# Kernel tuning notes

Measured on AMD Instinct MI355X. Metric: run time of the kernel, lower is better.

The kernel has to match this reference:

```python
import jax, jax.numpy as jnp
import numpy as np

L = 32      # num_layer
N_ORD = 64  # order_of_a_LTImodel
U = 64      # u_size
Y = 64      # y_size
T = 8192    # sequence length
SCALE = 0.05  # keep block-bidiagonal A spectrally stable over 8192 steps


def setup_inputs() -> dict:
    key = jax.random.key(0)
    k_u, k_a, k_b0, k_bl, k_c = jax.random.split(key, 5)
    inp = {
        "input": jax.random.normal(k_u, (T, U), dtype=jnp.float32),
        # per-layer A_i weights (diagonal blocks)
        "A_stack": jax.random.normal(k_a, (L, N_ORD, N_ORD), dtype=jnp.float32) * SCALE,
        # layer-0 B (maps u -> state)
        "B0": jax.random.normal(k_b0, (N_ORD, U), dtype=jnp.float32) * SCALE,
        # layer i>=1 B weights (sub-diagonal coupling blocks)
        "B_lower": jax.random.normal(k_bl, (L - 1, N_ORD, N_ORD), dtype=jnp.float32) * SCALE,
        # per-layer C_i weights, concatenated along columns in forward
        "C_stack": jax.random.normal(k_c, (L, Y, N_ORD), dtype=jnp.float32),
        # D is frozen zeros (feedthrough=False)
        "D_w": jnp.zeros((Y, U), dtype=jnp.float32),
    }
    return inp


def _assemble(A_stack, B0, B_lower, C_stack):
    l, n, _ = A_stack.shape
    S = l * n
    A = jnp.zeros((S, S), A_stack.dtype)
    for i in range(l):  # fixed small structural loop
        A = A.at[i * n:(i + 1) * n, i * n:(i + 1) * n].set(A_stack[i])
    for i in range(1, l):
        A = A.at[i * n:(i + 1) * n, (i - 1) * n:i * n].set(B_lower[i - 1])
    B = jnp.concatenate([B0, jnp.zeros((S - n, B0.shape[1]), B0.dtype)], axis=0)
    # torch.cat([C_i], dim=1): [Y, L*n]
    C = jnp.transpose(C_stack, (1, 0, 2)).reshape(C_stack.shape[1], S)
    return A, B, C


def reference(input, A_stack, B0, B_lower, C_stack, D_w):
    A, B, C = _assemble(A_stack, B0, B_lower, C_stack)
    S = A.shape[0]
    x0 = jnp.zeros((S,), input.dtype)

    def step(x, u):
        y = C @ x + D_w @ u      # output BEFORE state update (y_t uses x_t)
        x_next = A @ x + B @ u
        return x_next, y

    _, ys = jax.lax.scan(step, x0, input)
    return ys  # [T, Y]
```

## Files before the change

### kernel.cpp

```cpp
#include <hip/hip_runtime.h>


#define LYR 32
#define NO  64
#define TSEQ 8192
#define JT  16
#define KD  (JT*NO)
#define PROWS (TSEQ+JT)
#define PBUF ((size_t)PROWS*NO)
#define FD  4

typedef _Float16 h16;
typedef _Float16 h16x8 __attribute__((ext_vector_type(8)));
typedef float    f32x4 __attribute__((ext_vector_type(4)));

__global__ __launch_bounds__(256) void prep1(
    const float* __restrict__ u, const float* __restrict__ B0,
    const float* __restrict__ Bl, const float* __restrict__ Cst,
    h16* __restrict__ pall, h16* __restrict__ ccast, float* __restrict__ kf32)
{
    const int n_pad0 = JT*NO;
    const int n_u    = TSEQ*NO;
    const int n_c    = LYR*NO*NO;
    const int n_k    = LYR*NO*NO;
    const int n_zp   = 32*JT*NO;
    const int total8 = (n_pad0 + n_u + n_c + n_k + n_zp) >> 3;
    int idx8 = blockIdx.x*256 + threadIdx.x;
    const int4 zero4 = make_int4(0,0,0,0);
    for (; idx8 < total8; idx8 += gridDim.x*256) {
        int e = idx8 << 3;
        if (e < n_pad0) { *(int4*)&pall[e] = zero4; continue; }
        e -= n_pad0;
        if (e < n_u) {
            f32x4 f0 = *(const f32x4*)&u[e];
            f32x4 f1 = *(const f32x4*)&u[e+4];
            h16 ov[8];
            #pragma unroll
            for (int j = 0; j < 4; j++) { ov[j] = (h16)f0[j]; ov[4+j] = (h16)f1[j]; }
            *(int4*)&pall[n_pad0 + e] = *(int4*)&ov[0];
            continue;
        }
        e -= n_u;
        if (e < n_c) {
            f32x4 f0 = *(const f32x4*)&Cst[e];
            f32x4 f1 = *(const f32x4*)&Cst[e+4];
            h16 ov[8];
            #pragma unroll
            for (int j = 0; j < 4; j++) { ov[j] = (h16)f0[j]; ov[4+j] = (h16)f1[j]; }
            *(int4*)&ccast[e] = *(int4*)&ov[0];
            continue;
        }
        e -= n_c;
        if (e < n_k) {
            int i = e >> 12;
            int r = e & 4095;
            const float* src = (i == 0) ? &B0[r] : &Bl[e - 4096];
            float* dst = &kf32[((size_t)i*JT)*4096 + r];
            *(f32x4*)&dst[0] = *(const f32x4*)&src[0];
            *(f32x4*)&dst[4] = *(const f32x4*)&src[4];
            continue;
        }
        e -= n_k;
        int b = e >> 10;
        int off = e & 1023;
        *(int4*)&pall[(size_t)(b+1)*PBUF + off] = zero4;
    }
}

__global__ __launch_bounds__(256) void build_step(
    const float* __restrict__ A_stack, float* __restrict__ kf32,
    float* __restrict__ apow, int s)
{
    int h = 1 << s;
    int extra = (s < 3) ? 1 : 0;
    int slots = h + extra;
    int layer = blockIdx.x / slots;
    int q     = blockIdx.x % slots;
    const float* X = (s == 0) ? (A_stack + (size_t)layer*4096)
                              : (apow + ((size_t)layer*4 + (s-1))*4096);
    const float* Yop;
    float* Z;
    if (q < h) { Yop = kf32 + ((size_t)layer*JT + q)*4096;
                 Z   = kf32 + ((size_t)layer*JT + h + q)*4096; }
    else       { Yop = X;
                 Z   = apow + ((size_t)layer*4 + s)*4096; }

    __shared__ float lx[64*68];
    __shared__ float ly[64*68];
    int tid = threadIdx.x;
    for (int e = tid; e < 4096; e += 256) {
        int r = e >> 6, c = e & 63;
        lx[r*68 + c] = X[e];
        ly[r*68 + c] = Yop[e];
    }
    __syncthreads();
    int r0 = (tid >> 4) << 2;
    int c0 = (tid & 15) << 2;
    float acc[4][4] = {};
    for (int k = 0; k < 64; k++) {
        float a0 = lx[(r0+0)*68 + k];
        float a1 = lx[(r0+1)*68 + k];
        float a2 = lx[(r0+2)*68 + k];
        float a3 = lx[(r0+3)*68 + k];
        f32x4 bv = *(const f32x4*)&ly[k*68 + c0];
        #pragma unroll
        for (int j = 0; j < 4; j++) {
            acc[0][j] += a0*bv[j]; acc[1][j] += a1*bv[j];
            acc[2][j] += a2*bv[j]; acc[3][j] += a3*bv[j];
        }
    }
    #pragma unroll
    for (int i2 = 0; i2 < 4; i2++) {
        f32x4 o; o[0]=acc[i2][0]; o[1]=acc[i2][1]; o[2]=acc[i2][2]; o[3]=acc[i2][3];
        *(f32x4*)&Z[(size_t)(r0+i2)*64 + c0] = o;
    }
}

__global__ __launch_bounds__(256) void castK(const float* __restrict__ kf32,
                                             h16* __restrict__ kt)
{
    int idx4 = blockIdx.x*256 + threadIdx.x;
    const int total4 = (LYR*NO*KD) >> 2;
    for (; idx4 < total4; idx4 += gridDim.x*256) {
        int idx = idx4 << 2;
        int i   = idx >> 16;
        int rem = idx & 65535;
        int n   = rem >> 10;
        int kap = rem & 1023;
        int jp  = kap >> 6, m = kap & 63;
        int j   = JT-1-jp;
        f32x4 f = *(const f32x4*)&kf32[(((size_t)i*JT + j)*64 + n)*64 + m];
        h16 ov[4];
        #pragma unroll
        for (int t = 0; t < 4; t++) ov[t] = (h16)f[t];
        *(int2*)&kt[idx] = *(int2*)&ov[0];
    }
}

template<int S>
__device__ __forceinline__ void phase_body(
    const h16* inb, h16* outb, const h16* __restrict__ kb,
    h16* __restrict__ gout, const int w0, float* red, const int tid)
{
    const int wv = tid >> 6, lane = tid & 63, r = lane & 15, q = lane >> 4;
    const h16* abase = inb + (r + wv*4)*72 + q*8;
    const h16* bbase = kb + (size_t)r*KD + wv*256 + q*8;
#define LDA(s, ls) (*(const h16x8*)(abase + ((s)*16 + ((ls)>>1))*72 + ((ls)&1)*32))
#define LDB(c, ls) (*(const h16x8*)(bbase + (c)*(16*KD) + (ls)*32))
    f32x4 acc[S][4] = {};
    h16x8 a[2][S], b[4][4];
    #pragma unroll
    for (int ls = 0; ls < 2; ls++)
        #pragma unroll
        for (int s = 0; s < S; s++) a[ls][s] = LDA(s, ls);
    #pragma unroll
    for (int ls = 0; ls < 4; ls++)
        #pragma unroll
        for (int c = 0; c < 4; c++) b[ls][c] = LDB(c, ls);
    #pragma unroll
    for (int ls = 0; ls < 8; ls++) {
        h16x8 ca[S], cb[4];
        #pragma unroll
        for (int s = 0; s < S; s++) ca[s] = a[ls&1][s];
        #pragma unroll
        for (int c = 0; c < 4; c++) cb[c] = b[ls&3][c];
        if (ls < 6) {
            #pragma unroll
            for (int s = 0; s < S; s++) a[ls&1][s] = LDA(s, ls+2);
        }
        if (ls < 4) {
            #pragma unroll
            for (int c = 0; c < 4; c++) b[ls&3][c] = LDB(c, ls+4);
        }
        #pragma unroll
        for (int s = 0; s < S; s++)
            #pragma unroll
            for (int c = 0; c < 4; c++)
                acc[s][c] = __builtin_amdgcn_mfma_f32_16x16x32_f16(ca[s], cb[c], acc[s][c], 0,0,0);
    }
#undef LDA
#undef LDB
    const int cb2 = (tid & 7) << 3;
    #pragma unroll
    for (int ch = 0; ch < (S+2)/3; ch++) {
        const int sbase = ch*3;
        const int nt = (S - sbase) < 3 ? (S - sbase) : 3;
        __syncthreads();
        if (wv >= 2) {
            float* myred = red + (size_t)(wv-2)*(48*68);
            #pragma unroll
            for (int s2 = 0; s2 < 3; s2++) if (s2 < nt)
                #pragma unroll
                for (int c = 0; c < 4; c++)
                    #pragma unroll
                    for (int g = 0; g < 4; g++)
                        myred[(s2*16 + q*4 + g)*68 + c*16 + r] = acc[sbase+s2][c][g];
        }
        __syncthreads();
        if (wv < 2) {
            float* myred = red + (size_t)wv*(48*68);
            #pragma unroll
            for (int s2 = 0; s2 < 3; s2++) if (s2 < nt)
                #pragma unroll
                for (int c = 0; c < 4; c++)
                    #pragma unroll
                    for (int g = 0; g < 4; g++)
                        myred[(s2*16 + q*4 + g)*68 + c*16 + r] += acc[sbase+s2][c][g];
        }
        __syncthreads();
        for (int w = tid >> 3; w < nt*16; w += 32) {
            f32x4 u0 = *(const f32x4*)&red[w*68 + cb2];
            f32x4 u1 = *(const f32x4*)&red[w*68 + cb2 + 4];
            f32x4 v0 = *(const f32x4*)&red[48*68 + w*68 + cb2];
            f32x4 v1 = *(const f32x4*)&red[48*68 + w*68 + cb2 + 4];
            u0 += v0; u1 += v1;
            h16 ov[8];
            #pragma unroll
            for (int j = 0; j < 4; j++) { ov[j] = (h16)u0[j]; ov[4+j] = (h16)u1[j]; }
            const int W = sbase*16 + w;
            if (outb) *(int4*)&outb[W*72 + cb2] = *(int4*)&ov[0];
            const unsigned wrel = (unsigned)(W - w0);
            if (wrel < 32u) *(int4*)&gout[(size_t)wrel*64 + cb2] = *(int4*)&ov[0];
        }
    }
    __syncthreads();
}

__global__ __launch_bounds__(256) void stage4(
    h16* pall, const h16* __restrict__ kt, int i0)
{
    __shared__ __align__(16) h16   bufA[96*72];
    __shared__ __align__(16) h16   bufB[96*72];
    __shared__ __align__(16) float red[2*48*68];
    const int tid = threadIdx.x;
    const size_t t0 = (size_t)blockIdx.x * 32;

    const h16* pin = pall + (size_t)i0*PBUF;
    for (int e = tid; e < 96*8; e += 256) {
        int rr = e >> 3, cc = e & 7;
        long g = (long)t0 - 48 + rr;
        int4 v = make_int4(0,0,0,0);
        if (g >= 0) v = *(const int4*)&pin[(size_t)g*64 + cc*8];
        *(int4*)&bufA[rr*72 + cc*8] = v;
    }
    __syncthreads();

    h16* g1 = pall + (size_t)(i0+1)*PBUF + (JT + t0)*64;
    h16* g2 = pall + (size_t)(i0+2)*PBUF + (JT + t0)*64;
    h16* g3 = pall + (size_t)(i0+3)*PBUF + (JT + t0)*64;
    h16* g4 = pall + (size_t)(i0+4)*PBUF + (JT + t0)*64;
    const h16* k1 = kt + (size_t)(i0+0)*NO*KD;
    const h16* k2 = kt + (size_t)(i0+1)*NO*KD;
    const h16* k3 = kt + (size_t)(i0+2)*NO*KD;
    const h16* k4 = kt + (size_t)(i0+3)*NO*KD;

    phase_body<5>(bufA, bufB, k1, g1, 48, red, tid);
    phase_body<4>(bufB, bufA, k2, g2, 32, red, tid);
    phase_body<3>(bufA, bufB, k3, g3, 16, red, tid);
    phase_body<2>(bufB, (h16*)0, k4, g4, 0, red, tid);
}

__global__ __launch_bounds__(256, 2) void y_final(
    const h16* __restrict__ pall, const h16* __restrict__ ccast,
    float* __restrict__ out)
{
    __shared__ __align__(16) float red[2*32*68];
    int tid = threadIdx.x;
    size_t t0 = (size_t)blockIdx.x * 32;
    int wv = tid >> 6, lane = tid & 63, r = lane & 15, q = lane >> 4;
    const h16* abase = pall + (size_t)(wv*8 + 1)*PBUF + (JT + t0 + r)*64 + q*8;
    const h16* bbase = ccast + (size_t)(wv*8)*4096 + (size_t)r*64 + q*8;
#define LDA2(s, ls) (*(const h16x8*)(abase + (size_t)((ls)>>1)*PBUF + (s)*(16*64) + ((ls)&1)*32))
#define LDB2(c, ls) (*(const h16x8*)(bbase + ((ls)>>1)*4096 + (c)*(16*64) + ((ls)&1)*32))
    f32x4 acc[2][4] = {};
    h16x8 a[4][2], b[4][4];
    #pragma unroll
    for (int ls = 0; ls < 4; ls++) {
        #pragma unroll
        for (int s = 0; s < 2; s++) a[ls][s] = LDA2(s, ls);
        #pragma unroll
        for (int c = 0; c < 4; c++) b[ls][c] = LDB2(c, ls);
    }
    #pragma unroll
    for (int ls = 0; ls < 16; ls++) {
        h16x8 ca[2], cb[4];
        #pragma unroll
        for (int s = 0; s < 2; s++) ca[s] = a[ls&3][s];
        #pragma unroll
        for (int c = 0; c < 4; c++) cb[c] = b[ls&3][c];
        if (ls < 12) {
            #pragma unroll
            for (int s = 0; s < 2; s++) a[ls&3][s] = LDA2(s, ls+4);
            #pragma unroll
            for (int c = 0; c < 4; c++) b[ls&3][c] = LDB2(c, ls+4);
        }
        #pragma unroll
        for (int s = 0; s < 2; s++)
            #pragma unroll
            for (int c = 0; c < 4; c++)
                acc[s][c] = __builtin_amdgcn_mfma_f32_16x16x32_f16(ca[s], cb[c], acc[s][c], 0,0,0);
    }
#undef LDA2
#undef LDB2
    if (wv >= 2) {
        float* myred = red + (size_t)(wv-2)*(32*68);
        #pragma unroll
        for (int s = 0; s < 2; s++)
            #pragma unroll
            for (int c = 0; c < 4; c++)
                #pragma unroll
                for (int g = 0; g < 4; g++)
                    myred[(s*16 + q*4 + g)*68 + c*16 + r] = acc[s][c][g];
    }
    __syncthreads();
    if (wv < 2) {
        float* myred = red + (size_t)wv*(32*68);
        #pragma unroll
        for (int s = 0; s < 2; s++)
            #pragma unroll
            for (int c = 0; c < 4; c++)
                #pragma unroll
                for (int g = 0; g < 4; g++)
                    myred[(s*16 + q*4 + g)*68 + c*16 + r] += acc[s][c][g];
    }
    __syncthreads();
    int orow = tid >> 3, cb2 = (tid & 7) << 3;
    f32x4 u0 = *(const f32x4*)&red[orow*68 + cb2];
    f32x4 u1 = *(const f32x4*)&red[orow*68 + cb2 + 4];
    f32x4 v0 = *(const f32x4*)&red[32*68 + orow*68 + cb2];
    f32x4 v1 = *(const f32x4*)&red[32*68 + orow*68 + cb2 + 4];
    u0 += v0; u1 += v1;
    size_t obase = (t0 + orow)*64 + cb2;
    *(f32x4*)&out[obase]     = u0;
    *(f32x4*)&out[obase + 4] = u1;
}

extern "C" void kernel_launch(void* const* d_in, const int* in_sizes, int n_in,
                              void* d_out, int out_size, void* d_ws, size_t ws_size,
                              hipStream_t stream)
{
    const float* u   = (const float*)d_in[0];
    const float* Ast = (const float*)d_in[1];
    const float* B0  = (const float*)d_in[2];
    const float* Bl  = (const float*)d_in[3];
    const float* Cst = (const float*)d_in[4];
    float* out = (float*)d_out;
    (void)in_sizes; (void)n_in; (void)out_size; (void)ws_size;

    char* ws = (char*)d_ws;
    const size_t PBUF_BYTES = PBUF*sizeof(h16);
    h16*   pall  = (h16*)ws;
    h16*   ccast = (h16*)(ws + 33*PBUF_BYTES);
    h16*   kt    = (h16*)(ws + 33*PBUF_BYTES + 262144);
    float* kf32  = (float*)(ws + 33*PBUF_BYTES + 262144 + 4194304);
    float* apow  = (float*)(ws + 33*PBUF_BYTES + 262144 + 4194304 + 8388608);

    prep1<<<512, 256, 0, stream>>>(u, B0, Bl, Cst, pall, ccast, kf32);
    for (int s = 0; s < 4; s++) {
        int h = 1 << s;
        int grid = 32*(h + (s < 3 ? 1 : 0));
        build_step<<<grid, 256, 0, stream>>>(Ast, kf32, apow, s);
    }
    castK<<<2048, 256, 0, stream>>>(kf32, kt);
    for (int i = 0; i < LYR; i += FD) {
        stage4<<<TSEQ/32, 256, 0, stream>>>(pall, kt, i);
    }
    y_final<<<TSEQ/32, 256, 0, stream>>>(pall, ccast, out);
}
```

Baseline: 306.9 us.

## Halve time tile per block and fuse fp16 K-cast into last power step

Stage4 and y_final now process 16 timesteps per block instead of 32, doubling the grid, shrinking LDS buffers, and adding a two-blocks-per-SM launch bound so more waves stay resident. The fp16 cast and reversal of the impulse-response blocks moves into the final build_step launch, which removes the separate castK kernel. The catch is that the 48-row halo is now recomputed relative to a smaller useful tile, so redundant MFMA work per output row rises.

```diff
diff --git a/kernel.cpp b/kernel.cpp
--- a/kernel.cpp
+++ b/kernel.cpp
@@ -69,7 +69,7 @@
 
 __global__ __launch_bounds__(256) void build_step(
     const float* __restrict__ A_stack, float* __restrict__ kf32,
-    float* __restrict__ apow, int s)
+    float* __restrict__ apow, h16* __restrict__ kt, int s)
 {
     int h = 1 << s;
     int extra = (s < 3) ? 1 : 0;
@@ -109,31 +109,32 @@
             acc[2][j] += a2*bv[j]; acc[3][j] += a3*bv[j];
         }
     }
-    #pragma unroll
-    for (int i2 = 0; i2 < 4; i2++) {
-        f32x4 o; o[0]=acc[i2][0]; o[1]=acc[i2][1]; o[2]=acc[i2][2]; o[3]=acc[i2][3];
-        *(f32x4*)&Z[(size_t)(r0+i2)*64 + c0] = o;
-    }
-}
-
-__global__ __launch_bounds__(256) void castK(const float* __restrict__ kf32,
-                                             h16* __restrict__ kt)
-{
-    int idx4 = blockIdx.x*256 + threadIdx.x;
-    const int total4 = (LYR*NO*KD) >> 2;
-    for (; idx4 < total4; idx4 += gridDim.x*256) {
-        int idx = idx4 << 2;
-        int i   = idx >> 16;
-        int rem = idx & 65535;
-        int n   = rem >> 10;
-        int kap = rem & 1023;
-        int jp  = kap >> 6, m = kap & 63;
-        int j   = JT-1-jp;
-        f32x4 f = *(const f32x4*)&kf32[(((size_t)i*JT + j)*64 + n)*64 + m];
-        h16 ov[4];
-        #pragma unroll
-        for (int t = 0; t < 4; t++) ov[t] = (h16)f[t];
-        *(int2*)&kt[idx] = *(int2*)&ov[0];
+    if (s < 3) {
+        #pragma unroll
+        for (int i2 = 0; i2 < 4; i2++) {
+            f32x4 o; o[0]=acc[i2][0]; o[1]=acc[i2][1]; o[2]=acc[i2][2]; o[3]=acc[i2][3];
+            *(f32x4*)&Z[(size_t)(r0+i2)*64 + c0] = o;
+        }
+    } else {
+        size_t kb = (size_t)layer*65536 + (size_t)(7 - q)*64;
+        #pragma unroll
+        for (int i2 = 0; i2 < 4; i2++) {
+            h16 o4[4];
+            #pragma unroll
+            for (int j = 0; j < 4; j++) o4[j] = (h16)acc[i2][j];
+            *(int2*)&kt[kb + (size_t)(r0+i2)*1024 + c0] = *(int2*)&o4[0];
+        }
+        const float* Ksrc = kf32 + ((size_t)layer*JT + q)*4096;
+        size_t kb2 = (size_t)layer*65536 + (size_t)(15 - q)*64;
+        for (int g = tid; g < 1024; g += 256) {
+            int n  = g >> 4;
+            int m4 = (g & 15) << 2;
+            f32x4 f = *(const f32x4*)&Ksrc[(size_t)n*64 + m4];
+            h16 o4[4];
+            #pragma unroll
+            for (int t = 0; t < 4; t++) o4[t] = (h16)f[t];
+            *(int2*)&kt[kb2 + (size_t)n*1024 + m4] = *(int2*)&o4[0];
+        }
     }
 }
 
@@ -220,23 +221,23 @@
             const int W = sbase*16 + w;
             if (outb) *(int4*)&outb[W*72 + cb2] = *(int4*)&ov[0];
             const unsigned wrel = (unsigned)(W - w0);
-            if (wrel < 32u) *(int4*)&gout[(size_t)wrel*64 + cb2] = *(int4*)&ov[0];
-        }
-    }
-    __syncthreads();
-}
-
-__global__ __launch_bounds__(256) void stage4(
+            if (wrel < 16u) *(int4*)&gout[(size_t)wrel*64 + cb2] = *(int4*)&ov[0];
+        }
+    }
+    __syncthreads();
+}
+
+__global__ __launch_bounds__(256, 2) void stage4(
     h16* pall, const h16* __restrict__ kt, int i0)
 {
-    __shared__ __align__(16) h16   bufA[96*72];
-    __shared__ __align__(16) h16   bufB[96*72];
+    __shared__ __align__(16) h16   bufA[80*72];
+    __shared__ __align__(16) h16   bufB[80*72];
     __shared__ __align__(16) float red[2*48*68];
     const int tid = threadIdx.x;
-    const size_t t0 = (size_t)blockIdx.x * 32;
+    const size_t t0 = (size_t)blockIdx.x * 16;
 
     const h16* pin = pall + (size_t)i0*PBUF;
-    for (int e = tid; e < 96*8; e += 256) {
+    for (int e = tid; e < 80*8; e += 256) {
         int rr = e >> 3, cc = e & 7;
         long g = (long)t0 - 48 + rr;
         int4 v = make_int4(0,0,0,0);
@@ -254,85 +255,71 @@
     const h16* k3 = kt + (size_t)(i0+2)*NO*KD;
     const h16* k4 = kt + (size_t)(i0+3)*NO*KD;
 
-    phase_body<5>(bufA, bufB, k1, g1, 48, red, tid);
-    phase_body<4>(bufB, bufA, k2, g2, 32, red, tid);
-    phase_body<3>(bufA, bufB, k3, g3, 16, red, tid);
-    phase_body<2>(bufB, (h16*)0, k4, g4, 0, red, tid);
+    phase_body<4>(bufA, bufB, k1, g1, 48, red, tid);
+    phase_body<3>(bufB, bufA, k2, g2, 32, red, tid);
+    phase_body<2>(bufA, bufB, k3, g3, 16, red, tid);
+    phase_body<1>(bufB, (h16*)0, k4, g4, 0, red, tid);
 }
 
 __global__ __launch_bounds__(256, 2) void y_final(
     const h16* __restrict__ pall, const h16* __restrict__ ccast,
     float* __restrict__ out)
 {
-    __shared__ __align__(16) float red[2*32*68];
+    __shared__ __align__(16) float red[2*16*68];
     int tid = threadIdx.x;
-    size_t t0 = (size_t)blockIdx.x * 32;
+    size_t t0 = (size_t)blockIdx.x * 16;
     int wv = tid >> 6, lane = tid & 63, r = lane & 15, q = lane >> 4;
     const h16* abase = pall + (size_t)(wv*8 + 1)*PBUF + (JT + t0 + r)*64 + q*8;
     const h16* bbase = ccast + (size_t)(wv*8)*4096 + (size_t)r*64 + q*8;
-#define LDA2(s, ls) (*(const h16x8*)(abase + (size_t)((ls)>>1)*PBUF + (s)*(16*64) + ((ls)&1)*32))
+#define LDA2(ls) (*(const h16x8*)(abase + (size_t)((ls)>>1)*PBUF + ((ls)&1)*32))
 #define LDB2(c, ls) (*(const h16x8*)(bbase + ((ls)>>1)*4096 + (c)*(16*64) + ((ls)&1)*32))
-    f32x4 acc[2][4] = {};
-    h16x8 a[4][2], b[4][4];
+    f32x4 acc[4] = {};
+    h16x8 a[4], b[4][4];
     #pragma unroll
     for (int ls = 0; ls < 4; ls++) {
-        #pragma unroll
-        for (int s = 0; s < 2; s++) a[ls][s] = LDA2(s, ls);
+        a[ls] = LDA2(ls);
         #pragma unroll
         for (int c = 0; c < 4; c++) b[ls][c] = LDB2(c, ls);
     }
     #pragma unroll
     for (int ls = 0; ls < 16; ls++) {
-        h16x8 ca[2], cb[4];
-        #pragma unroll
-        for (int s = 0; s < 2; s++) ca[s] = a[ls&3][s];
+        h16x8 ca = a[ls&3], cb[4];
         #pragma unroll
         for (int c = 0; c < 4; c++) cb[c] = b[ls&3][c];
         if (ls < 12) {
-            #pragma unroll
-            for (int s = 0; s < 2; s++) a[ls&3][s] = LDA2(s, ls+4);
+            a[ls&3] = LDA2(ls+4);
             #pragma unroll
             for (int c = 0; c < 4; c++) b[ls&3][c] = LDB2(c, ls+4);
         }
         #pragma unroll
-        for (int s = 0; s < 2; s++)
-            #pragma unroll
-            for (int c = 0; c < 4; c++)
-                acc[s][c] = __builtin_amdgcn_mfma_f32_16x16x32_f16(ca[s], cb[c], acc[s][c], 0,0,0);
+        for (int c = 0; c < 4; c++)
+            acc[c] = __builtin_amdgcn_mfma_f32_16x16x32_f16(ca, cb[c], acc[c], 0,0,0);
     }
 #undef LDA2
 #undef LDB2
     if (wv >= 2) {
-        float* myred = red + (size_t)(wv-2)*(32*68);
-        #pragma unroll
-        for (int s = 0; s < 2; s++)
-            #pragma unroll
-            for (int c = 0; c < 4; c++)
-                #pragma unroll
-                for (int g = 0; g < 4; g++)
-                    myred[(s*16 + q*4 + g)*68 + c*16 + r] = acc[s][c][g];
+        float* myred = red + (size_t)(wv-2)*(16*68);
+        #pragma unroll
+        for (int c = 0; c < 4; c++)
+            #pragma unroll
+            for (int g = 0; g < 4; g++)
+                myred[(q*4 + g)*68 + c*16 + r] = acc[c][g];
     }
     __syncthreads();
     if (wv < 2) {
-        float* myred = red + (size_t)wv*(32*68);
-        #pragma unroll
-        for (int s = 0; s < 2; s++)
-            #pragma unroll
-            for (int c = 0; c < 4; c++)
-                #pragma unroll
-                for (int g = 0; g < 4; g++)
-                    myred[(s*16 + q*4 + g)*68 + c*16 + r] += acc[s][c][g];
-    }
-    __syncthreads();
-    int orow = tid >> 3, cb2 = (tid & 7) << 3;
-    f32x4 u0 = *(const f32x4*)&red[orow*68 + cb2];
-    f32x4 u1 = *(const f32x4*)&red[orow*68 + cb2 + 4];
-    f32x4 v0 = *(const f32x4*)&red[32*68 + orow*68 + cb2];
-    f32x4 v1 = *(const f32x4*)&red[32*68 + orow*68 + cb2 + 4];
-    u0 += v0; u1 += v1;
-    size_t obase = (t0 + orow)*64 + cb2;
-    *(f32x4*)&out[obase]     = u0;
-    *(f32x4*)&out[obase + 4] = u1;
+        float* myred = red + (size_t)wv*(16*68);
+        #pragma unroll
+        for (int c = 0; c < 4; c++)
+            #pragma unroll
+            for (int g = 0; g < 4; g++)
+                myred[(q*4 + g)*68 + c*16 + r] += acc[c][g];
+    }
+    __syncthreads();
+    int orow = tid >> 4, c4 = (tid & 15) << 2;
+    f32x4 u0 = *(const f32x4*)&red[orow*68 + c4];
+    f32x4 v0 = *(const f32x4*)&red[16*68 + orow*68 + c4];
+    u0 += v0;
+    *(f32x4*)&out[(t0 + orow)*64 + c4] = u0;
 }
 
 extern "C" void kernel_launch(void* const* d_in, const int* in_sizes, int n_in,
@@ -359,11 +346,10 @@
     for (int s = 0; s < 4; s++) {
         int h = 1 << s;
         int grid = 32*(h + (s < 3 ? 1 : 0));
-        build_step<<<grid, 256, 0, stream>>>(Ast, kf32, apow, s);
-    }
-    castK<<<2048, 256, 0, stream>>>(kf32, kt);
+        build_step<<<grid, 256, 0, stream>>>(Ast, kf32, apow, kt, s);
+    }
     for (int i = 0; i < LYR; i += FD) {
-        stage4<<<TSEQ/32, 256, 0, stream>>>(pall, kt, i);
-    }
-    y_final<<<TSEQ/32, 256, 0, stream>>>(pall, ccast, out);
-}
+        stage4<<<TSEQ/16, 256, 0, stream>>>(pall, kt, i);
+    }
+    y_final<<<TSEQ/16, 256, 0, stream>>>(pall, ccast, out);
+}
```

Result: slower. 376.1 us (+22.5%).

## Fuse kernel-power build into prep and fuse two layers per stage launch

Applied to the files above, without the earlier changes.

Replaces the four doubling build_step launches and the castK pass with one prep_build kernel. In it, 32 blocks each compute A^j*B for j=1..15 sequentially in shared memory and write fp16 kt directly, while the remaining blocks do the input and C casts and zero-padding. The layer stage now fuses 2 layers per launch instead of 4. That doubles the stage launch count but shrinks the halo recomputation (16 instead of 48 rows) and the shared-memory footprint. The sequential power chain in only 32 blocks may lengthen prep, and more launches add overhead.

```diff
diff --git a/kernel.cpp b/kernel.cpp
--- a/kernel.cpp
+++ b/kernel.cpp
@@ -8,26 +8,83 @@
 #define KD  (JT*NO)
 #define PROWS (TSEQ+JT)
 #define PBUF ((size_t)PROWS*NO)
-#define FD  4
 
 typedef _Float16 h16;
 typedef _Float16 h16x8 __attribute__((ext_vector_type(8)));
 typedef float    f32x4 __attribute__((ext_vector_type(4)));
 
-__global__ __launch_bounds__(256) void prep1(
+__global__ __launch_bounds__(256) void prep_build(
     const float* __restrict__ u, const float* __restrict__ B0,
     const float* __restrict__ Bl, const float* __restrict__ Cst,
-    h16* __restrict__ pall, h16* __restrict__ ccast, float* __restrict__ kf32)
-{
+    const float* __restrict__ Ast,
+    h16* __restrict__ pall, h16* __restrict__ ccast, h16* __restrict__ kt)
+{
+    __shared__ float sm[3*64*68];
+    const int tid = threadIdx.x;
+
+    if (blockIdx.x < 32) {
+        const int layer = blockIdx.x;
+        float* la = sm;
+        float* kc = sm + 64*68;
+        float* kn = sm + 2*64*68;
+        const float* k0 = (layer == 0) ? B0 : (Bl + (size_t)(layer-1)*4096);
+        const float* Aw = Ast + (size_t)layer*4096;
+        for (int e = tid; e < 4096; e += 256) {
+            int r = e >> 6, c = e & 63;
+            kc[r*68 + c] = k0[e];
+            la[r*68 + c] = Aw[e];
+        }
+        __syncthreads();
+        {
+            size_t kb = (size_t)layer*65536 + 15*64;
+            for (int e2 = tid; e2 < 1024; e2 += 256) {
+                int n = e2 >> 4, c4 = (e2 & 15) << 2;
+                h16 o4[4];
+                #pragma unroll
+                for (int t = 0; t < 4; t++) o4[t] = (h16)kc[n*68 + c4 + t];
+                *(int2*)&kt[kb + (size_t)n*1024 + c4] = *(int2*)&o4[0];
+            }
+        }
+        const int r0 = (tid >> 4) << 2;
+        const int c0 = (tid & 15) << 2;
+        for (int j = 1; j <= 15; j++) {
+            float acc[4][4] = {};
+            for (int k = 0; k < 64; k++) {
+                float a0 = la[(r0+0)*68 + k];
+                float a1 = la[(r0+1)*68 + k];
+                float a2 = la[(r0+2)*68 + k];
+                float a3 = la[(r0+3)*68 + k];
+                f32x4 bv = *(const f32x4*)&kc[k*68 + c0];
+                #pragma unroll
+                for (int jj = 0; jj < 4; jj++) {
+                    acc[0][jj] += a0*bv[jj]; acc[1][jj] += a1*bv[jj];
+                    acc[2][jj] += a2*bv[jj]; acc[3][jj] += a3*bv[jj];
+                }
+            }
+            size_t kb = (size_t)layer*65536 + (size_t)(15 - j)*64;
+            #pragma unroll
+            for (int i2 = 0; i2 < 4; i2++) {
+                f32x4 o; o[0]=acc[i2][0]; o[1]=acc[i2][1]; o[2]=acc[i2][2]; o[3]=acc[i2][3];
+                *(f32x4*)&kn[(r0+i2)*68 + c0] = o;
+                h16 o4[4];
+                #pragma unroll
+                for (int t = 0; t < 4; t++) o4[t] = (h16)acc[i2][t];
+                *(int2*)&kt[kb + (size_t)(r0+i2)*1024 + c0] = *(int2*)&o4[0];
+            }
+            __syncthreads();
+            float* tmp = kc; kc = kn; kn = tmp;
+        }
+        return;
+    }
+
     const int n_pad0 = JT*NO;
     const int n_u    = TSEQ*NO;
     const int n_c    = LYR*NO*NO;
-    const int n_k    = LYR*NO*NO;
     const int n_zp   = 32*JT*NO;
-    const int total8 = (n_pad0 + n_u + n_c + n_k + n_zp) >> 3;
-    int idx8 = blockIdx.x*256 + threadIdx.x;
+    const int total8 = (n_pad0 + n_u + n_c + n_zp) >> 3;
+    int idx8 = (blockIdx.x - 32)*256 + tid;
     const int4 zero4 = make_int4(0,0,0,0);
-    for (; idx8 < total8; idx8 += gridDim.x*256) {
+    for (; idx8 < total8; idx8 += 512*256) {
         int e = idx8 << 3;
         if (e < n_pad0) { *(int4*)&pall[e] = zero4; continue; }
         e -= n_pad0;
@@ -51,89 +108,9 @@
             continue;
         }
         e -= n_c;
-        if (e < n_k) {
-            int i = e >> 12;
-            int r = e & 4095;
-            const float* src = (i == 0) ? &B0[r] : &Bl[e - 4096];
-            float* dst = &kf32[((size_t)i*JT)*4096 + r];
-            *(f32x4*)&dst[0] = *(const f32x4*)&src[0];
-            *(f32x4*)&dst[4] = *(const f32x4*)&src[4];
-            continue;
-        }
-        e -= n_k;
         int b = e >> 10;
         int off = e & 1023;
         *(int4*)&pall[(size_t)(b+1)*PBUF + off] = zero4;
-    }
-}
-
-__global__ __launch_bounds__(256) void build_step(
-    const float* __restrict__ A_stack, float* __restrict__ kf32,
-    float* __restrict__ apow, int s)
-{
-    int h = 1 << s;
-    int extra = (s < 3) ? 1 : 0;
-    int slots = h + extra;
-    int layer = blockIdx.x / slots;
-    int q     = blockIdx.x % slots;
-    const float* X = (s == 0) ? (A_stack + (size_t)layer*4096)
-                              : (apow + ((size_t)layer*4 + (s-1))*4096);
-    const float* Yop;
-    float* Z;
-    if (q < h) { Yop = kf32 + ((size_t)layer*JT + q)*4096;
-                 Z   = kf32 + ((size_t)layer*JT + h + q)*4096; }
-    else       { Yop = X;
-                 Z   = apow + ((size_t)layer*4 + s)*4096; }
-
-    __shared__ float lx[64*68];
-    __shared__ float ly[64*68];
-    int tid = threadIdx.x;
-    for (int e = tid; e < 4096; e += 256) {
-        int r = e >> 6, c = e & 63;
-        lx[r*68 + c] = X[e];
-        ly[r*68 + c] = Yop[e];
-    }
-    __syncthreads();
-    int r0 = (tid >> 4) << 2;
-    int c0 = (tid & 15) << 2;
-    float acc[4][4] = {};
-    for (int k = 0; k < 64; k++) {
-        float a0 = lx[(r0+0)*68 + k];
-        float a1 = lx[(r0+1)*68 + k];
-        float a2 = lx[(r0+2)*68 + k];
-        float a3 = lx[(r0+3)*68 + k];
-        f32x4 bv = *(const f32x4*)&ly[k*68 + c0];
-        #pragma unroll
-        for (int j = 0; j < 4; j++) {
-            acc[0][j] += a0*bv[j]; acc[1][j] += a1*bv[j];
-            acc[2][j] += a2*bv[j]; acc[3][j] += a3*bv[j];
-        }
-    }
-    #pragma unroll
-    for (int i2 = 0; i2 < 4; i2++) {
-        f32x4 o; o[0]=acc[i2][0]; o[1]=acc[i2][1]; o[2]=acc[i2][2]; o[3]=acc[i2][3];
-        *(f32x4*)&Z[(size_t)(r0+i2)*64 + c0] = o;
-    }
-}
-
-__global__ __launch_bounds__(256) void castK(const float* __restrict__ kf32,
-                                             h16* __restrict__ kt)
-{
-    int idx4 = blockIdx.x*256 + threadIdx.x;
-    const int total4 = (LYR*NO*KD) >> 2;
-    for (; idx4 < total4; idx4 += gridDim.x*256) {
-        int idx = idx4 << 2;
-        int i   = idx >> 16;
-        int rem = idx & 65535;
-        int n   = rem >> 10;
-        int kap = rem & 1023;
-        int jp  = kap >> 6, m = kap & 63;
-        int j   = JT-1-jp;
-        f32x4 f = *(const f32x4*)&kf32[(((size_t)i*JT + j)*64 + n)*64 + m];
-        h16 ov[4];
-        #pragma unroll
-        for (int t = 0; t < 4; t++) ov[t] = (h16)f[t];
-        *(int2*)&kt[idx] = *(int2*)&ov[0];
     }
 }
 
@@ -226,19 +203,19 @@
     __syncthreads();
 }
 
-__global__ __launch_bounds__(256) void stage4(
+__global__ __launch_bounds__(256) void stage2(
     h16* pall, const h16* __restrict__ kt, int i0)
 {
-    __shared__ __align__(16) h16   bufA[96*72];
-    __shared__ __align__(16) h16   bufB[96*72];
+    __shared__ __align__(16) h16   bufA[64*72];
+    __shared__ __align__(16) h16   bufB[48*72];
     __shared__ __align__(16) float red[2*48*68];
     const int tid = threadIdx.x;
     const size_t t0 = (size_t)blockIdx.x * 32;
 
     const h16* pin = pall + (size_t)i0*PBUF;
-    for (int e = tid; e < 96*8; e += 256) {
+    for (int e = tid; e < 64*8; e += 256) {
         int rr = e >> 3, cc = e & 7;
-        long g = (long)t0 - 48 + rr;
+        long g = (long)t0 - 16 + rr;
         int4 v = make_int4(0,0,0,0);
         if (g >= 0) v = *(const int4*)&pin[(size_t)g*64 + cc*8];
         *(int4*)&bufA[rr*72 + cc*8] = v;
@@ -247,17 +224,11 @@
 
     h16* g1 = pall + (size_t)(i0+1)*PBUF + (JT + t0)*64;
     h16* g2 = pall + (size_t)(i0+2)*PBUF + (JT + t0)*64;
-    h16* g3 = pall + (size_t)(i0+3)*PBUF + (JT + t0)*64;
-    h16* g4 = pall + (size_t)(i0+4)*PBUF + (JT + t0)*64;
     const h16* k1 = kt + (size_t)(i0+0)*NO*KD;
     const h16* k2 = kt + (size_t)(i0+1)*NO*KD;
-    const h16* k3 = kt + (size_t)(i0+2)*NO*KD;
-    const h16* k4 = kt + (size_t)(i0+3)*NO*KD;
-
-    phase_body<5>(bufA, bufB, k1, g1, 48, red, tid);
-    phase_body<4>(bufB, bufA, k2, g2, 32, red, tid);
-    phase_body<3>(bufA, bufB, k3, g3, 16, red, tid);
-    phase_body<2>(bufB, (h16*)0, k4, g4, 0, red, tid);
+
+    phase_body<3>(bufA, bufB, k1, g1, 16, red, tid);
+    phase_body<2>(bufB, (h16*)0, k2, g2, 0, red, tid);
 }
 
 __global__ __launch_bounds__(256, 2) void y_final(
@@ -352,18 +323,10 @@
     h16*   pall  = (h16*)ws;
     h16*   ccast = (h16*)(ws + 33*PBUF_BYTES);
     h16*   kt    = (h16*)(ws + 33*PBUF_BYTES + 262144);
-    float* kf32  = (float*)(ws + 33*PBUF_BYTES + 262144 + 4194304);
-    float* apow  = (float*)(ws + 33*PBUF_BYTES + 262144 + 4194304 + 8388608);
-
-    prep1<<<512, 256, 0, stream>>>(u, B0, Bl, Cst, pall, ccast, kf32);
-    for (int s = 0; s < 4; s++) {
-        int h = 1 << s;
-        int grid = 32*(h + (s < 3 ? 1 : 0));
-        build_step<<<grid, 256, 0, stream>>>(Ast, kf32, apow, s);
-    }
-    castK<<<2048, 256, 0, stream>>>(kf32, kt);
-    for (int i = 0; i < LYR; i += FD) {
-        stage4<<<TSEQ/32, 256, 0, stream>>>(pall, kt, i);
+
+    prep_build<<<544, 256, 0, stream>>>(u, B0, Bl, Cst, Ast, pall, ccast, kt);
+    for (int i = 0; i < LYR; i += 2) {
+        stage2<<<TSEQ/32, 256, 0, stream>>>(pall, kt, i);
     }
     y_final<<<TSEQ/32, 256, 0, stream>>>(pall, ccast, out);
 }
```

Measured after the change: 317.9 us. 1.04x slower.
